# Performance work log

Hardware: AMD Instinct MI355X
Metric: run time of the kernel (lower is better)

## Reference

```python
import jax, jax.numpy as jnp
import numpy as np

N = 8192      # points
K = 16        # nsample neighbors
CIN = 64      # in_plane
C = 256       # out_plane (== mid_planes)
S = 8         # share_planes
EPS = 1e-5


def _bn(x, g, b, axes):
    # BatchNorm1d (training-mode batch stats, biased var), channel = last dim
    m = x.mean(axes, keepdims=True)
    v = x.var(axes, keepdims=True)
    return (x - m) / jnp.sqrt(v + EPS) * g + b


def _knn(p, k):
    # brute-force KNN over a single batch (o = [N]); indices include self
    sq = jnp.sum(p * p, axis=1)
    d2 = sq[:, None] + sq[None, :] - 2.0 * (p @ p.T)   # [N, N]
    idx = jax.lax.top_k(-d2, k)[1]                      # [N, K]
    return jax.lax.stop_gradient(idx)


def setup_inputs() -> dict:
    key = jax.random.key(0)
    ks = jax.random.split(key, 16)
    W = lambda i, shp, s=0.05: jax.random.normal(ks[i], shp, jnp.float32) * s
    one = lambda d: jnp.ones((d,), jnp.float32)
    zero = lambda d: jnp.zeros((d,), jnp.float32)
    return {
        "p": jax.random.normal(ks[0], (N, 3), jnp.float32),
        "x": jax.random.normal(ks[1], (N, CIN), jnp.float32),
        "o": jnp.array([N], dtype=jnp.int32),
        # PointAggregation (stride=1): Linear(no bias) + BN
        "W_pa": W(2, (CIN, C)), "g_pa": one(C), "b_pa": zero(C),
        # SelfFusion.linear1 (no bias) + bn1
        "W1": W(3, (C, C)), "g1": one(C), "b1": zero(C),
        # SelfFusionLayer q/k/v
        "Wq": W(4, (C, C)), "bq": zero(C),
        "Wk": W(5, (C, C)), "bk": zero(C),
        "Wv": W(6, (C, C)), "bv": zero(C),
        # linear_p: Linear(3,3)+BN(3)+ReLU+Linear(3,C)
        "Wp1": W(7, (3, 3), 0.3), "bp1": zero(3), "gp": one(3), "bp": zero(3),
        "Wp2": W(8, (3, C), 0.3), "bp2": zero(C),
        # linear_w: BN(C)+ReLU+Linear(C,C//S)+BN(C//S)+ReLU+Linear(C//S,C//S)
        "gw1": one(C), "bw1": zero(C),
        "Ww1": W(9, (C, C // S)), "bww1": zero(C // S),
        "gw2": one(C // S), "bw2": zero(C // S),
        "Ww2": W(10, (C // S, C // S), 0.2), "bww2": zero(C // S),
        # bn2, linear3 (no bias) + bn3
        "g2": one(C), "b2": zero(C),
        "W3": W(11, (C, C)), "g3": one(C), "b3": zero(C),
    }


def reference(p, x, o, W_pa, g_pa, b_pa, W1, g1, b1, Wq, bq, Wk, bk, Wv, bv,
              Wp1, bp1, gp, bp, Wp2, bp2, gw1, bw1, Ww1, bww1, gw2, bw2,
              Ww2, bww2, g2, b2, W3, g3, b3):
    relu = jax.nn.relu
    # --- PointAggregation (stride=1) ---
    h = relu(_bn(x @ W_pa, g_pa, b_pa, (0,)))          # [N, C]
    # --- SelfFusion block ---
    identity = h
    h = relu(_bn(h @ W1, g1, b1, (0,)))                # [N, C]
    # SelfFusionLayer
    xq = h @ Wq + bq                                   # [N, C]
    xk = h @ Wk + bk
    xv = h @ Wv + bv
    idx = _knn(p, K)                                   # [N, K]
    rel = p[idx] - p[:, None, :]                       # [N, K, 3] relative coords
    xk_g = xk[idx]                                     # [N, K, C]
    xv_g = xv[idx]                                     # [N, K, C]
    # linear_p: Linear(3,3) -> BN(3) -> ReLU -> Linear(3,C)
    p_r = rel @ Wp1 + bp1
    p_r = relu(_bn(p_r, gp, bp, (0, 1)))
    p_r = p_r @ Wp2 + bp2                              # [N, K, C]
    # mid_planes == out_planes so view(...).sum(2) is identity
    w = xk_g - xq[:, None, :] + p_r                    # [N, K, C]
    # linear_w: BN -> ReLU -> Linear -> BN -> ReLU -> Linear
    w = relu(_bn(w, gw1, bw1, (0, 1)))
    w = w @ Ww1 + bww1                                 # [N, K, C//S]
    w = relu(_bn(w, gw2, bw2, (0, 1)))
    w = w @ Ww2 + bww2                                 # [N, K, C//S]
    w = jax.nn.softmax(w, axis=1)                      # softmax over neighbors
    y = ((xv_g + p_r).reshape(N, K, S, C // S) * w[:, :, None, :]).sum(1)
    y = y.reshape(N, C)
    # back in SelfFusion
    y = relu(_bn(y, g2, b2, (0,)))
    y = _bn(y @ W3, g3, b3, (0,))
    x2 = relu(y + identity)
    return (p, x2, o)
```

## Files before the change

kernel.cpp:

```cpp
#include <hip/hip_runtime.h>
#include <hip/hip_bf16.h>

#define INV_N  (1.0f/8192.0f)
#define INV_NK (1.0f/131072.0f)

typedef __attribute__((ext_vector_type(8))) short bf16x8;
typedef __attribute__((ext_vector_type(4))) float f32x4;
typedef unsigned short u16;

__device__ __forceinline__ u16 f2b(float f) {
  unsigned u = __float_as_uint(f);
  return (u16)((u + 0x7FFFu + ((u >> 16) & 1u)) >> 16);
}
__device__ __forceinline__ float b2f(u16 u) {
  return __uint_as_float(((unsigned)u) << 16);
}

__device__ __forceinline__ float bn_ap(float v, const float* st, int C, int ch,
                                       float inv, float g, float b) {
  float m = st[ch] * inv;
  float var = st[C + ch] * inv - m * m;
  return (v - m) * rsqrtf(var + 1e-5f) * g + b;
}

__launch_bounds__(256)
__global__ void prep_k(const float* __restrict__ p, const int* __restrict__ o,
                       const float* __restrict__ Ww1,
                       float4* __restrict__ pp, u16* __restrict__ Ww1t,
                       float* __restrict__ st, float* __restrict__ out) {
  int b = blockIdx.x, t = threadIdx.x;
  int e = b*256 + t;
  if (b < 16) st[b*256 + t] = 0.f;
  if (e < 24576) out[e] = p[e];
  if (e == 0) out[24576 + 2097152] = (float)o[0];
  if (e < 8192) {
    float x = p[e*3+0], y = p[e*3+1], z = p[e*3+2];
    pp[e] = make_float4(x, y, z, (x*x + y*y) + z*z);
  }
  if (b >= 88) {
    int q = (b - 88)*1024 + t*4;
#pragma unroll
    for (int ii = 0; ii < 4; ++ii) {
      int e2 = q + ii;
      int k = e2 >> 5, n = e2 & 31;
      Ww1t[n*256 + k] = f2b(Ww1[e2]);
    }
  }
}

template<int ROWS, int SPLIT>
__launch_bounds__(256)
__global__ void red_k(const float* __restrict__ part, float* __restrict__ outp,
                      int width) {
  int ncg = width >> 6;
  int cg = blockIdx.x % ncg, sp = blockIdx.x / ncg;
  int lane = threadIdx.x & 63, chunk = threadIdx.x >> 6;
  int c = cg*64 + lane;
  constexpr int R  = ROWS / SPLIT;
  constexpr int RC = R / 4;
  float s = 0.f;
  int i0 = sp*R + chunk*RC;
#pragma unroll 4
  for (int i = i0; i < i0 + RC; ++i) s += part[(size_t)i*width + c];
  __shared__ float red[4][64];
  red[chunk][lane] = s;
  __syncthreads();
  if (threadIdx.x < 64) {
    float v = red[0][lane] + red[1][lane] + red[2][lane] + red[3][lane];
    if (SPLIT == 1) outp[c] = v;
    else atomicAdd(&outp[c], v);
  }
}

__launch_bounds__(512)
__global__ void knn_k(const float4* __restrict__ pp, int* __restrict__ idxo) {
  __shared__ float4 buf[2048];
  int t = threadIdx.x;
  int wave = t >> 6, lane = t & 63;
  int q = blockIdx.x*8 + wave;
  float4 qv = pp[q];
  const float BIG = __uint_as_float(0x7F7FFFFFu);
  float d[3];
#pragma unroll
  for (int s = 0; s < 3; ++s) d[s] = BIG;
  for (int ch = 0; ch < 4; ++ch) {
#pragma unroll
    for (int s = 0; s < 4; ++s)
      buf[s*512 + t] = pp[ch*2048 + s*512 + t];
    __syncthreads();
#pragma unroll 4
    for (int it = 0; it < 32; ++it) {
      int jl = it*64 + lane;
      float4 c = buf[jl];
      int j = ch*2048 + jl;
      float dot = qv.x*c.x + (qv.y*c.y + qv.z*c.z);
      float d2 = __fmaf_rn(-2.0f, dot, qv.w + c.w);
      float pk = __uint_as_float((__float_as_uint(d2) & 0xFFFFE000u) | (unsigned)j);
      d[2] = fminf(fmaxf(d[1], pk), d[2]);
      d[1] = fminf(fmaxf(d[0], pk), d[1]);
      d[0] = fminf(d[0], pk);
    }
    __syncthreads();
  }
  for (int r = 0; r < 16; ++r) {
    float bd = d[0];
#pragma unroll
    for (int m = 1; m < 64; m <<= 1)
      bd = fminf(bd, __shfl_xor(bd, m));
    if (lane == 0) idxo[q*16 + r] = (int)(__float_as_uint(bd) & 0x1FFFu);
    if (d[0] == bd) {
      d[0] = d[1]; d[1] = d[2]; d[2] = BIG;
    }
  }
}

template<typename TA, typename TO, bool BNA, bool STATS>
__launch_bounds__(256)
__global__ void mfgemm_k(const TA* __restrict__ A, const float* __restrict__ st,
                         const float* __restrict__ g, const float* __restrict__ bb,
                         float inv_cnt,
                         const float* __restrict__ W, TO* __restrict__ out,
                         float* __restrict__ stout, int KA, int NOUT) {
  __shared__ short As[64][72];
  __shared__ short Bt[64][72];
  __shared__ float lscl[256], lsft[256];
  int t = threadIdx.x;
  int m0 = blockIdx.x * 64, n0 = blockIdx.y * 64;
  if (BNA) {
    for (int e = t; e < KA; e += 256) {
      float m = st[e] * inv_cnt;
      float var = st[KA + e] * inv_cnt - m*m;
      float sc = rsqrtf(var + 1e-5f) * g[e];
      lscl[e] = sc; lsft[e] = bb[e] - m*sc;
    }
    __syncthreads();
  }
  const f32x4 zero = {0.f, 0.f, 0.f, 0.f};
  f32x4 acc[2][2] = {{zero, zero}, {zero, zero}};
  int wv = t >> 6, l = t & 63;
  int wm = wv & 1, wn = wv >> 1;
  int lr = l & 15, lk = (l >> 4) * 8;
  int ra = t >> 4, qa = t & 15;
  int bn = t & 63, bkc = t >> 6;
  for (int k0 = 0; k0 < KA; k0 += 64) {
#pragma unroll
    for (int rp = 0; rp < 4; ++rp) {
      int r = rp*16 + ra;
      float vv[4];
      if constexpr (sizeof(TA) == 4) {
        float4 av = *(const float4*)((const float*)A + (size_t)(m0 + r)*KA + k0 + qa*4);
        vv[0] = av.x; vv[1] = av.y; vv[2] = av.z; vv[3] = av.w;
      } else {
        short4 av = *(const short4*)((const u16*)A + (size_t)(m0 + r)*KA + k0 + qa*4);
#pragma unroll
        for (int jj = 0; jj < 4; ++jj) vv[jj] = b2f(((u16*)&av)[jj]);
      }
      short4 s;
#pragma unroll
      for (int jj = 0; jj < 4; ++jj) {
        float v = vv[jj];
        if (BNA) { int ch = k0 + qa*4 + jj; v = fmaxf(fmaf(v, lscl[ch], lsft[ch]), 0.f); }
        ((u16*)&s)[jj] = f2b(v);
      }
      *(short4*)&As[r][qa*4] = s;
    }
    {
      float v[16];
#pragma unroll
      for (int j2 = 0; j2 < 16; ++j2)
        v[j2] = W[(size_t)(k0 + bkc*16 + j2)*NOUT + n0 + bn];
      bf16x8 w0, w1v;
#pragma unroll
      for (int j2 = 0; j2 < 8; ++j2) {
        w0[j2]  = (short)f2b(v[j2]);
        w1v[j2] = (short)f2b(v[8 + j2]);
      }
      *(bf16x8*)&Bt[bn][bkc*16]     = w0;
      *(bf16x8*)&Bt[bn][bkc*16 + 8] = w1v;
    }
    __syncthreads();
#pragma unroll
    for (int fk = 0; fk < 2; ++fk) {
      bf16x8 a0 = *(const bf16x8*)&As[wm*32 +      lr][fk*32 + lk];
      bf16x8 a1 = *(const bf16x8*)&As[wm*32 + 16 + lr][fk*32 + lk];
      bf16x8 b0 = *(const bf16x8*)&Bt[wn*32 +      lr][fk*32 + lk];
      bf16x8 b1 = *(const bf16x8*)&Bt[wn*32 + 16 + lr][fk*32 + lk];
      acc[0][0] = __builtin_amdgcn_mfma_f32_16x16x32_bf16(a0, b0, acc[0][0], 0, 0, 0);
      acc[0][1] = __builtin_amdgcn_mfma_f32_16x16x32_bf16(a0, b1, acc[0][1], 0, 0, 0);
      acc[1][0] = __builtin_amdgcn_mfma_f32_16x16x32_bf16(a1, b0, acc[1][0], 0, 0, 0);
      acc[1][1] = __builtin_amdgcn_mfma_f32_16x16x32_bf16(a1, b1, acc[1][1], 0, 0, 0);
    }
    __syncthreads();
  }
#pragma unroll
  for (int fn = 0; fn < 2; ++fn) {
    int col = n0 + wn*32 + fn*16 + lr;
    float s1 = 0.f, s2 = 0.f;
#pragma unroll
    for (int fm = 0; fm < 2; ++fm) {
#pragma unroll
      for (int r = 0; r < 4; ++r) {
        int row = m0 + wm*32 + fm*16 + (l >> 4)*4 + r;
        float v = acc[fm][fn][r];
        if constexpr (sizeof(TO) == 4) out[(size_t)row*NOUT + col] = v;
        else                           out[(size_t)row*NOUT + col] = f2b(v);
        if (STATS) { s1 += v; s2 += v*v; }
      }
    }
    if (STATS) {
      s1 += __shfl_xor(s1, 16); s1 += __shfl_xor(s1, 32);
      s2 += __shfl_xor(s2, 16); s2 += __shfl_xor(s2, 32);
      if (l < 16) {
        atomicAdd(&stout[col], s1);
        atomicAdd(&stout[NOUT + col], s2);
      }
    }
  }
}

__launch_bounds__(256)
__global__ void qkv_k(const u16* __restrict__ t1, const float* __restrict__ st,
                      const float* __restrict__ g1, const float* __restrict__ b1,
                      const float* __restrict__ Wq, const float* __restrict__ bq,
                      const float* __restrict__ Wk, const float* __restrict__ bk,
                      const float* __restrict__ Wv, const float* __restrict__ bv,
                      u16* __restrict__ xq, u16* __restrict__ xk, u16* __restrict__ xv) {
  __shared__ short As[64][72];
  __shared__ short Bt[3][64][72];
  __shared__ float lscl[256], lsft[256];
  int t = threadIdx.x;
  int m0 = blockIdx.x * 64, n0 = blockIdx.y * 64;
  {
    int e = t;
    float m = st[e] * INV_N;
    float var = st[256 + e] * INV_N - m*m;
    float sc = rsqrtf(var + 1e-5f) * g1[e];
    lscl[e] = sc; lsft[e] = b1[e] - m*sc;
  }
  __syncthreads();
  const f32x4 zero = {0.f, 0.f, 0.f, 0.f};
  f32x4 acc[3][2][2];
#pragma unroll
  for (int w = 0; w < 3; ++w)
#pragma unroll
    for (int i = 0; i < 2; ++i)
#pragma unroll
      for (int j = 0; j < 2; ++j) acc[w][i][j] = zero;
  int wv = t >> 6, l = t & 63;
  int wm = wv & 1, wn = wv >> 1;
  int lr = l & 15, lk = (l >> 4) * 8;
  int ra = t >> 4, qa = t & 15;
  int bn = t & 63, bkc = t >> 6;
  const float* Ws[3] = {Wq, Wk, Wv};
  for (int k0 = 0; k0 < 256; k0 += 64) {
#pragma unroll
    for (int rp = 0; rp < 4; ++rp) {
      int r = rp*16 + ra;
      short4 av = *(const short4*)(t1 + (size_t)(m0 + r)*256 + k0 + qa*4);
      short4 s;
#pragma unroll
      for (int jj = 0; jj < 4; ++jj) {
        int ch = k0 + qa*4 + jj;
        float v = fmaxf(fmaf(b2f(((u16*)&av)[jj]), lscl[ch], lsft[ch]), 0.f);
        ((u16*)&s)[jj] = f2b(v);
      }
      *(short4*)&As[r][qa*4] = s;
    }
#pragma unroll
    for (int w = 0; w < 3; ++w) {
      float v[16];
#pragma unroll
      for (int j2 = 0; j2 < 16; ++j2)
        v[j2] = Ws[w][(size_t)(k0 + bkc*16 + j2)*256 + n0 + bn];
      bf16x8 w0, w1v;
#pragma unroll
      for (int j2 = 0; j2 < 8; ++j2) {
        w0[j2]  = (short)f2b(v[j2]);
        w1v[j2] = (short)f2b(v[8 + j2]);
      }
      *(bf16x8*)&Bt[w][bn][bkc*16]     = w0;
      *(bf16x8*)&Bt[w][bn][bkc*16 + 8] = w1v;
    }
    __syncthreads();
#pragma unroll
    for (int fk = 0; fk < 2; ++fk) {
      bf16x8 a0 = *(const bf16x8*)&As[wm*32 +      lr][fk*32 + lk];
      bf16x8 a1 = *(const bf16x8*)&As[wm*32 + 16 + lr][fk*32 + lk];
#pragma unroll
      for (int w = 0; w < 3; ++w) {
        bf16x8 b0 = *(const bf16x8*)&Bt[w][wn*32 +      lr][fk*32 + lk];
        bf16x8 b1 = *(const bf16x8*)&Bt[w][wn*32 + 16 + lr][fk*32 + lk];
        acc[w][0][0] = __builtin_amdgcn_mfma_f32_16x16x32_bf16(a0, b0, acc[w][0][0], 0, 0, 0);
        acc[w][0][1] = __builtin_amdgcn_mfma_f32_16x16x32_bf16(a0, b1, acc[w][0][1], 0, 0, 0);
        acc[w][1][0] = __builtin_amdgcn_mfma_f32_16x16x32_bf16(a1, b0, acc[w][1][0], 0, 0, 0);
        acc[w][1][1] = __builtin_amdgcn_mfma_f32_16x16x32_bf16(a1, b1, acc[w][1][1], 0, 0, 0);
      }
    }
    __syncthreads();
  }
  u16* outs[3] = {xq, xk, xv};
  const float* bs[3] = {bq, bk, bv};
#pragma unroll
  for (int w = 0; w < 3; ++w) {
#pragma unroll
    for (int fn = 0; fn < 2; ++fn) {
      int col = n0 + wn*32 + fn*16 + lr;
      float bvv = bs[w][col];
#pragma unroll
      for (int fm = 0; fm < 2; ++fm) {
#pragma unroll
        for (int r = 0; r < 4; ++r) {
          int row = m0 + wm*32 + fm*16 + (l >> 4)*4 + r;
          outs[w][(size_t)row*256 + col] = f2b(acc[w][fm][fn][r] + bvv);
        }
      }
    }
  }
}

__launch_bounds__(256)
__global__ void stats256_k(const u16* __restrict__ X, float* __restrict__ psy) {
  int c = threadIdx.x;
  int r0 = blockIdx.x * 32;
  float s1 = 0.f, s2 = 0.f;
  for (int r = 0; r < 32; ++r) {
    float v = b2f(X[(size_t)(r0 + r)*256 + c]);
    s1 += v; s2 += v*v;
  }
  psy[(size_t)blockIdx.x*512 + c]       = s1;
  psy[(size_t)blockIdx.x*512 + 256 + c] = s2;
}

__device__ __forceinline__ void comp_pr1(const float* p, int i, int j,
                                         const float* Wp1, const float* bp1,
                                         float pr1[3]) {
  float rx = p[j*3+0] - p[i*3+0];
  float ry = p[j*3+1] - p[i*3+1];
  float rz = p[j*3+2] - p[i*3+2];
#pragma unroll
  for (int c = 0; c < 3; ++c)
    pr1[c] = rx*Wp1[c] + ry*Wp1[3+c] + rz*Wp1[6+c] + bp1[c];
}

__device__ __forceinline__ void comp_prv(const float* p, int i, int j,
                                         const float* Wp1, const float* bp1,
                                         const float* gp, const float* bpp,
                                         const float* sp, float o3[3]) {
  float pr1[3];
  comp_pr1(p, i, j, Wp1, bp1, pr1);
#pragma unroll
  for (int c = 0; c < 3; ++c)
    o3[c] = fmaxf(bn_ap(pr1[c], sp, 3, c, INV_NK, gp[c], bpp[c]), 0.0f);
}

__launch_bounds__(256)
__global__ void prstats_k(const float* __restrict__ p, const int* __restrict__ idx,
                          const float* Wp1, const float* bp1, float* __restrict__ sp) {
  float s[3] = {0,0,0}, s2[3] = {0,0,0};
  for (int it = 0; it < 4; ++it) {
    int e = blockIdx.x*1024 + it*256 + threadIdx.x;
    int i = e >> 4;
    int j = idx[e] & 8191;
    float pr1[3];
    comp_pr1(p, i, j, Wp1, bp1, pr1);
#pragma unroll
    for (int c = 0; c < 3; ++c) { s[c] += pr1[c]; s2[c] += pr1[c]*pr1[c]; }
  }
#pragma unroll
  for (int m = 1; m < 64; m <<= 1) {
#pragma unroll
    for (int c = 0; c < 3; ++c) {
      s[c]  += __shfl_xor(s[c],  m);
      s2[c] += __shfl_xor(s2[c], m);
    }
  }
  __shared__ float red[4][6];
  int wv = threadIdx.x >> 6, lane = threadIdx.x & 63;
  if (lane == 0) {
#pragma unroll
    for (int c = 0; c < 3; ++c) { red[wv][c] = s[c]; red[wv][3+c] = s2[c]; }
  }
  __syncthreads();
  if (threadIdx.x < 6) {
    float v = red[0][threadIdx.x] + red[1][threadIdx.x] +
              red[2][threadIdx.x] + red[3][threadIdx.x];
    atomicAdd(&sp[threadIdx.x], v);
  }
}

__launch_bounds__(256)
__global__ void wstats_k(const u16* __restrict__ xk, const u16* __restrict__ xq,
                         const float* __restrict__ p, const int* __restrict__ idx,
                         const float* Wp1, const float* bp1, const float* gp, const float* bpp,
                         const float* sp, const float* __restrict__ Wp2, const float* bp2,
                         float* __restrict__ pws) {
  __shared__ float prv[8][16][4];
  __shared__ int   jidx[8][16];
  int base = blockIdx.x * 8;
  int t = threadIdx.x;
  if (t < 128) {
    int pt = t >> 4, k = t & 15;
    int j = idx[(base + pt)*16 + k] & 8191;
    jidx[pt][k] = j;
    float o3[3];
    comp_prv(p, base + pt, j, Wp1, bp1, gp, bpp, sp, o3);
    prv[pt][k][0] = o3[0]; prv[pt][k][1] = o3[1]; prv[pt][k][2] = o3[2];
  }
  __syncthreads();
  int c = t;
  float wp0 = Wp2[c], wp1v = Wp2[256+c], wp2v = Wp2[512+c];
  float bbv = bp2[c];
  float s1 = 0.f, s2 = 0.f;
  for (int pt = 0; pt < 8; ++pt) {
    int i = base + pt;
    float xqv = b2f(xq[(size_t)i*256 + c]);
    u16 kvals[16];
#pragma unroll
    for (int k = 0; k < 16; ++k)
      kvals[k] = xk[(size_t)jidx[pt][k]*256 + c];
#pragma unroll
    for (int k = 0; k < 16; ++k) {
      float pr = prv[pt][k][0]*wp0 + prv[pt][k][1]*wp1v + prv[pt][k][2]*wp2v + bbv;
      float wval = b2f(kvals[k]) - xqv + pr;
      s1 += wval; s2 += wval*wval;
    }
  }
  pws[(size_t)blockIdx.x*512 + c]       = s1;
  pws[(size_t)blockIdx.x*512 + 256 + c] = s2;
}

__launch_bounds__(256)
__global__ void w1gemm_k(const u16* __restrict__ xk, const u16* __restrict__ xq,
                         const float* __restrict__ p, const int* __restrict__ idx,
                         const float* Wp1, const float* bp1, const float* gp, const float* bpp,
                         const float* sp, const float* __restrict__ Wp2, const float* bp2,
                         const float* sw, const float* gw1, const float* bw1,
                         const u16* __restrict__ Ww1t, const float* bww1,
                         u16* __restrict__ w1, float* __restrict__ pw1) {
  __shared__ short sA[64][264];
  __shared__ float prv[64][3];
  __shared__ int   jrow[64];
  __shared__ float sred[256];
  int t = threadIdx.x;
  int base4 = blockIdx.x * 4;
  if (t < 64) {
    int grow = blockIdx.x*64 + t;
    int j = idx[grow] & 8191;
    jrow[t] = j;
    float o3[3];
    comp_prv(p, grow >> 4, j, Wp1, bp1, gp, bpp, sp, o3);
    prv[t][0] = o3[0]; prv[t][1] = o3[1]; prv[t][2] = o3[2];
  }
  __syncthreads();
  {
    int o = t & 31, rs = t >> 5;
    int ch0 = o*8;
    int jr[8];
#pragma unroll
    for (int ii = 0; ii < 8; ++ii) jr[ii] = jrow[ii*8 + rs];
    bf16x8 kvv[8], qvv[8];
#pragma unroll
    for (int ii = 0; ii < 8; ++ii) {
      int r = ii*8 + rs;
      kvv[ii] = *(const bf16x8*)(xk + (size_t)jr[ii]*256 + ch0);
      qvv[ii] = *(const bf16x8*)(xq + (size_t)(base4 + (r >> 4))*256 + ch0);
    }
    float sclv[8], sftv[8], w0v[8], w1vv[8], w2v[8], b2v[8];
#pragma unroll
    for (int h = 0; h < 2; ++h) {
      float4 swm = *(const float4*)(sw + ch0 + h*4);
      float4 sws = *(const float4*)(sw + 256 + ch0 + h*4);
      float4 g4  = *(const float4*)(gw1 + ch0 + h*4);
      float4 bb4 = *(const float4*)(bw1 + ch0 + h*4);
      float4 p0v = *(const float4*)(Wp2 + ch0 + h*4);
      float4 p1v = *(const float4*)(Wp2 + 256 + ch0 + h*4);
      float4 p2v = *(const float4*)(Wp2 + 512 + ch0 + h*4);
      float4 bp4 = *(const float4*)(bp2 + ch0 + h*4);
      float mv[4] = {swm.x, swm.y, swm.z, swm.w};
      float sv[4] = {sws.x, sws.y, sws.z, sws.w};
      float gv[4] = {g4.x, g4.y, g4.z, g4.w};
      float bv[4] = {bb4.x, bb4.y, bb4.z, bb4.w};
      float a0[4] = {p0v.x, p0v.y, p0v.z, p0v.w};
      float a1[4] = {p1v.x, p1v.y, p1v.z, p1v.w};
      float a2[4] = {p2v.x, p2v.y, p2v.z, p2v.w};
      float a3[4] = {bp4.x, bp4.y, bp4.z, bp4.w};
#pragma unroll
      for (int jj = 0; jj < 4; ++jj) {
        int e = h*4 + jj;
        float m = mv[jj]*INV_NK;
        float var = sv[jj]*INV_NK - m*m;
        float sc = rsqrtf(var + 1e-5f)*gv[jj];
        sclv[e] = sc; sftv[e] = bv[jj] - m*sc;
        w0v[e] = a0[jj]; w1vv[e] = a1[jj]; w2v[e] = a2[jj]; b2v[e] = a3[jj];
      }
    }
#pragma unroll
    for (int ii = 0; ii < 8; ++ii) {
      int r = ii*8 + rs;
      float p0 = prv[r][0], p1 = prv[r][1], p2 = prv[r][2];
      bf16x8 av;
#pragma unroll
      for (int e = 0; e < 8; ++e) {
        float v = b2f((u16)kvv[ii][e]) - b2f((u16)qvv[ii][e])
                + p0*w0v[e] + p1*w1vv[e] + p2*w2v[e] + b2v[e];
        v = fmaxf(fmaf(v, sclv[e], sftv[e]), 0.f);
        av[e] = (short)f2b(v);
      }
      *(bf16x8*)&sA[r][ch0] = av;
    }
  }
  __syncthreads();
  const f32x4 zero = {0.f,0.f,0.f,0.f};
  f32x4 acc[2] = {zero, zero};
  int wv = t >> 6, l = t & 63;
  int lr = l & 15, hi = l >> 4;
#pragma unroll
  for (int k0 = 0; k0 < 8; ++k0) {
    int kb = k0*32 + hi*8;
    bf16x8 a  = *(const bf16x8*)&sA[wv*16 + lr][kb];
    bf16x8 b0 = *(const bf16x8*)(Ww1t + (size_t)lr*256      + kb);
    bf16x8 b1 = *(const bf16x8*)(Ww1t + (size_t)(16+lr)*256 + kb);
    acc[0] = __builtin_amdgcn_mfma_f32_16x16x32_bf16(a, b0, acc[0], 0, 0, 0);
    acc[1] = __builtin_amdgcn_mfma_f32_16x16x32_bf16(a, b1, acc[1], 0, 0, 0);
  }
#pragma unroll
  for (int fn = 0; fn < 2; ++fn) {
    int col = fn*16 + lr;
    float bv = bww1[col];
    float s1 = 0.f, s2 = 0.f;
#pragma unroll
    for (int r = 0; r < 4; ++r) {
      int grow = blockIdx.x*64 + wv*16 + hi*4 + r;
      float v = acc[fn][r] + bv;
      w1[(size_t)grow*32 + col] = f2b(v);
      s1 += v; s2 += v*v;
    }
    s1 += __shfl_xor(s1, 16); s1 += __shfl_xor(s1, 32);
    s2 += __shfl_xor(s2, 16); s2 += __shfl_xor(s2, 32);
    if (l < 16) { sred[(wv*2+fn)*16 + lr] = s1; sred[128 + (wv*2+fn)*16 + lr] = s2; }
  }
  __syncthreads();
  if (t < 32) {
    float a = 0.f, b = 0.f;
#pragma unroll
    for (int w2 = 0; w2 < 4; ++w2) {
      a += sred[(w2*2 + (t >> 4))*16 + (t & 15)];
      b += sred[128 + (w2*2 + (t >> 4))*16 + (t & 15)];
    }
    pw1[(size_t)blockIdx.x*64 + t]      = a;
    pw1[(size_t)blockIdx.x*64 + 32 + t] = b;
  }
}

__launch_bounds__(256)
__global__ void aggr_k(const u16* __restrict__ w1, const float* sw1,
                       const float* gw2, const float* bw2,
                       const float* __restrict__ Ww2, const float* bww2,
                       const u16* __restrict__ xv,
                       const float* __restrict__ p, const int* __restrict__ idx,
                       const float* Wp1, const float* bp1, const float* gp, const float* bpp,
                       const float* sp, const float* __restrict__ Wp2, const float* bp2,
                       u16* __restrict__ y) {
  __shared__ float lw1[16][32];
  __shared__ float lW2[32][32];
  __shared__ float sw2[16][33];
  __shared__ float prv[16][4];
  __shared__ int   jidx[16];
  int i = blockIdx.x, t = threadIdx.x;
  for (int e = t; e < 1024; e += 256) lW2[e >> 5][e & 31] = Ww2[e];
  for (int e = t; e < 512; e += 256) {
    int c32 = e & 31;
    float v = b2f(w1[(size_t)i*512 + e]);
    v = fmaxf(bn_ap(v, sw1, 32, c32, INV_NK, gw2[c32], bw2[c32]), 0.0f);
    lw1[e >> 5][c32] = v;
  }
  if (t < 16) jidx[t] = idx[i*16 + t] & 8191;
  __syncthreads();
  if (t < 16) {
    float o3[3];
    comp_prv(p, i, jidx[t], Wp1, bp1, gp, bpp, sp, o3);
    prv[t][0] = o3[0]; prv[t][1] = o3[1]; prv[t][2] = o3[2];
  }
  for (int e = t; e < 512; e += 256) {
    int k = e >> 5, c32 = e & 31;
    float a = bww2[c32];
#pragma unroll
    for (int j = 0; j < 32; ++j) a += lw1[k][j] * lW2[j][c32];
    sw2[k][c32] = a;
  }
  __syncthreads();
  if (t < 32) {
    float mx = -3.0e38f;
#pragma unroll
    for (int k = 0; k < 16; ++k) mx = fmaxf(mx, sw2[k][t]);
    float s = 0.f;
#pragma unroll
    for (int k = 0; k < 16; ++k) { float e2 = expf(sw2[k][t] - mx); sw2[k][t] = e2; s += e2; }
    float r = 1.0f / s;
#pragma unroll
    for (int k = 0; k < 16; ++k) sw2[k][t] *= r;
  }
  __syncthreads();
  int c = t;
  float wp0 = Wp2[c], wp1v = Wp2[256+c], wp2v = Wp2[512+c];
  float bbv = bp2[c];
  int c32 = c & 31;
  float acc = 0.f;
#pragma unroll
  for (int k = 0; k < 16; ++k) {
    int j = jidx[k];
    float pr = prv[k][0]*wp0 + prv[k][1]*wp1v + prv[k][2]*wp2v + bbv;
    float xvv = b2f(xv[(size_t)j*256 + c]);
    acc += (xvv + pr) * sw2[k][c32];
  }
  y[(size_t)i*256 + c] = f2b(acc);
}

__launch_bounds__(256)
__global__ void final_k(const u16* __restrict__ t0, const float* s0,
                        const float* g0, const float* b0,
                        const u16* __restrict__ t3, const float* s3,
                        const float* g3, const float* b3,
                        float* __restrict__ out) {
  int i = blockIdx.x, c = threadIdx.x;
  size_t off = (size_t)i*256 + c;
  float h0 = fmaxf(bn_ap(b2f(t0[off]), s0, 256, c, INV_N, g0[c], b0[c]), 0.0f);
  float v3 = bn_ap(b2f(t3[off]), s3, 256, c, INV_N, g3[c], b3[c]);
  out[24576 + off] = fmaxf(v3 + h0, 0.0f);
}

extern "C" void kernel_launch(void* const* d_in, const int* in_sizes, int n_in,
                              void* d_out, int out_size, void* d_ws, size_t ws_size,
                              hipStream_t stream) {
  (void)in_sizes; (void)n_in; (void)out_size; (void)ws_size;
  const float* p    = (const float*)d_in[0];
  const float* x    = (const float*)d_in[1];
  const int*   o    = (const int*)  d_in[2];
  const float* W_pa = (const float*)d_in[3];
  const float* g_pa = (const float*)d_in[4];
  const float* b_pa = (const float*)d_in[5];
  const float* W1   = (const float*)d_in[6];
  const float* g1   = (const float*)d_in[7];
  const float* b1   = (const float*)d_in[8];
  const float* Wq   = (const float*)d_in[9];
  const float* bq   = (const float*)d_in[10];
  const float* Wk   = (const float*)d_in[11];
  const float* bk   = (const float*)d_in[12];
  const float* Wv   = (const float*)d_in[13];
  const float* bv   = (const float*)d_in[14];
  const float* Wp1  = (const float*)d_in[15];
  const float* bp1  = (const float*)d_in[16];
  const float* gp   = (const float*)d_in[17];
  const float* bpp  = (const float*)d_in[18];
  const float* Wp2  = (const float*)d_in[19];
  const float* bp2  = (const float*)d_in[20];
  const float* gw1  = (const float*)d_in[21];
  const float* bw1  = (const float*)d_in[22];
  const float* Ww1  = (const float*)d_in[23];
  const float* bww1 = (const float*)d_in[24];
  const float* gw2  = (const float*)d_in[25];
  const float* bw2  = (const float*)d_in[26];
  const float* Ww2  = (const float*)d_in[27];
  const float* bww2 = (const float*)d_in[28];
  const float* g2   = (const float*)d_in[29];
  const float* b2   = (const float*)d_in[30];
  const float* W3   = (const float*)d_in[31];
  const float* g3   = (const float*)d_in[32];
  const float* b3   = (const float*)d_in[33];

  char* ws = (char*)d_ws;
  u16*   t0  = (u16*)  (ws + 0);
  u16*   t1  = (u16*)  (ws + 4194304);
  u16*   xq  = (u16*)  (ws + 8388608);
  u16*   xk  = (u16*)  (ws + 12582912);
  u16*   xv  = (u16*)  (ws + 16777216);
  u16*   w1  = (u16*)  (ws + 20971520);
  int*   idx = (int*)  (ws + 29360128);
  float* st  = (float*)(ws + 29884416);
  u16*   Ww1t= (u16*)  (ws + 29900800);
  float* pw1 = (float*)(ws + 30408704);
  float* pws = (float*)(ws + 30932992);
  float* psy = (float*)(ws + 33030144);
  u16*   y   = t1;
  u16*   t3  = xq;
  float4* pp = (float4*)(ws + 20971520);

  prep_k<<<96, 256, 0, stream>>>(p, o, Ww1, pp, Ww1t, st, (float*)d_out);
  knn_k<<<1024, 512, 0, stream>>>(pp, idx);

  mfgemm_k<float, u16, false, true><<<dim3(128, 4), 256, 0, stream>>>(
      x, nullptr, nullptr, nullptr, 0.f, W_pa, t0, st + 0, 64, 256);

  mfgemm_k<u16, u16, true, true><<<dim3(128, 4), 256, 0, stream>>>(
      t0, st + 0, g_pa, b_pa, INV_N, W1, t1, st + 512, 256, 256);

  qkv_k<<<dim3(128, 4), 256, 0, stream>>>(
      t1, st + 512, g1, b1, Wq, bq, Wk, bk, Wv, bv, xq, xk, xv);

  prstats_k<<<128, 256, 0, stream>>>(p, idx, Wp1, bp1, st + 2624);

  wstats_k<<<1024, 256, 0, stream>>>(xk, xq, p, idx, Wp1, bp1, gp, bpp,
                                     st + 2624, Wp2, bp2, pws);
  red_k<1024, 4><<<32, 256, 0, stream>>>(pws, st + 1024, 512);

  w1gemm_k<<<2048, 256, 0, stream>>>(xk, xq, p, idx, Wp1, bp1, gp, bpp,
                                     st + 2624, Wp2, bp2, st + 1024,
                                     gw1, bw1, Ww1t, bww1, w1, pw1);
  red_k<2048, 16><<<16, 256, 0, stream>>>(pw1, st + 2560, 64);

  aggr_k<<<8192, 256, 0, stream>>>(w1, st + 2560, gw2, bw2, Ww2, bww2, xv,
                                   p, idx, Wp1, bp1, gp, bpp, st + 2624,
                                   Wp2, bp2, y);
  stats256_k<<<256, 256, 0, stream>>>(y, psy);
  red_k<256, 2><<<16, 256, 0, stream>>>(psy, st + 1536, 512);

  mfgemm_k<u16, u16, true, true><<<dim3(128, 4), 256, 0, stream>>>(
      y, st + 1536, g2, b2, INV_N, W3, t3, st + 2048, 256, 256);

  final_k<<<8192, 256, 0, stream>>>(t0, st + 0, g_pa, b_pa,
                                    t3, st + 2048, g3, b3, (float*)d_out);
}
```

Before: 198.0 us.

## Fuse independent KNN and first GEMM into one launch, and prstats with second GEMM

```diff
diff --git a/kernel.cpp b/kernel.cpp
--- a/kernel.cpp
+++ b/kernel.cpp
@@ -72,12 +72,12 @@
   }
 }
 
-__launch_bounds__(512)
-__global__ void knn_k(const float4* __restrict__ pp, int* __restrict__ idxo) {
-  __shared__ float4 buf[2048];
+__device__ __forceinline__ void knn_dev(char* smem, const float4* __restrict__ pp,
+                                        int* __restrict__ idxo, int kb) {
+  float4* buf = (float4*)smem;
   int t = threadIdx.x;
   int wave = t >> 6, lane = t & 63;
-  int q = blockIdx.x*8 + wave;
+  int q = kb*4 + wave;
   float4 qv = pp[q];
   const float BIG = __uint_as_float(0x7F7FFFFFu);
   float d[3];
@@ -85,8 +85,8 @@
   for (int s = 0; s < 3; ++s) d[s] = BIG;
   for (int ch = 0; ch < 4; ++ch) {
 #pragma unroll
-    for (int s = 0; s < 4; ++s)
-      buf[s*512 + t] = pp[ch*2048 + s*512 + t];
+    for (int s = 0; s < 8; ++s)
+      buf[s*256 + t] = pp[ch*2048 + s*256 + t];
     __syncthreads();
 #pragma unroll 4
     for (int it = 0; it < 32; ++it) {
@@ -115,17 +115,17 @@
 }
 
 template<typename TA, typename TO, bool BNA, bool STATS>
-__launch_bounds__(256)
-__global__ void mfgemm_k(const TA* __restrict__ A, const float* __restrict__ st,
-                         const float* __restrict__ g, const float* __restrict__ bb,
-                         float inv_cnt,
-                         const float* __restrict__ W, TO* __restrict__ out,
-                         float* __restrict__ stout, int KA, int NOUT) {
-  __shared__ short As[64][72];
-  __shared__ short Bt[64][72];
-  __shared__ float lscl[256], lsft[256];
+__device__ __forceinline__ void mfgemm_dev(char* smem,
+    const TA* __restrict__ A, const float* __restrict__ st,
+    const float* __restrict__ g, const float* __restrict__ bb, float inv_cnt,
+    const float* __restrict__ W, TO* __restrict__ out,
+    float* __restrict__ stout, int KA, int NOUT, int bm, int bn_) {
+  short (*As)[72] = (short(*)[72])smem;
+  short (*Bt)[72] = (short(*)[72])(smem + 9216);
+  float* lscl = (float*)(smem + 18432);
+  float* lsft = (float*)(smem + 19456);
   int t = threadIdx.x;
-  int m0 = blockIdx.x * 64, n0 = blockIdx.y * 64;
+  int m0 = bm * 64, n0 = bn_ * 64;
   if (BNA) {
     for (int e = t; e < KA; e += 256) {
       float m = st[e] * inv_cnt;
@@ -216,6 +216,105 @@
       }
     }
   }
+}
+
+__device__ __forceinline__ void comp_pr1(const float* p, int i, int j,
+                                         const float* Wp1, const float* bp1,
+                                         float pr1[3]) {
+  float rx = p[j*3+0] - p[i*3+0];
+  float ry = p[j*3+1] - p[i*3+1];
+  float rz = p[j*3+2] - p[i*3+2];
+#pragma unroll
+  for (int c = 0; c < 3; ++c)
+    pr1[c] = rx*Wp1[c] + ry*Wp1[3+c] + rz*Wp1[6+c] + bp1[c];
+}
+
+__device__ __forceinline__ void comp_prv(const float* p, int i, int j,
+                                         const float* Wp1, const float* bp1,
+                                         const float* gp, const float* bpp,
+                                         const float* sp, float o3[3]) {
+  float pr1[3];
+  comp_pr1(p, i, j, Wp1, bp1, pr1);
+#pragma unroll
+  for (int c = 0; c < 3; ++c)
+    o3[c] = fmaxf(bn_ap(pr1[c], sp, 3, c, INV_NK, gp[c], bpp[c]), 0.0f);
+}
+
+__device__ __forceinline__ void prstats_dev(char* smem,
+    const float* __restrict__ p, const int* __restrict__ idx,
+    const float* Wp1, const float* bp1, float* __restrict__ sp, int pb) {
+  float s[3] = {0,0,0}, s2[3] = {0,0,0};
+  for (int it = 0; it < 4; ++it) {
+    int e = pb*1024 + it*256 + threadIdx.x;
+    int i = e >> 4;
+    int j = idx[e] & 8191;
+    float pr1[3];
+    comp_pr1(p, i, j, Wp1, bp1, pr1);
+#pragma unroll
+    for (int c = 0; c < 3; ++c) { s[c] += pr1[c]; s2[c] += pr1[c]*pr1[c]; }
+  }
+#pragma unroll
+  for (int m = 1; m < 64; m <<= 1) {
+#pragma unroll
+    for (int c = 0; c < 3; ++c) {
+      s[c]  += __shfl_xor(s[c],  m);
+      s2[c] += __shfl_xor(s2[c], m);
+    }
+  }
+  float (*red)[6] = (float(*)[6])smem;
+  int wv = threadIdx.x >> 6, lane = threadIdx.x & 63;
+  if (lane == 0) {
+#pragma unroll
+    for (int c = 0; c < 3; ++c) { red[wv][c] = s[c]; red[wv][3+c] = s2[c]; }
+  }
+  __syncthreads();
+  if (threadIdx.x < 6) {
+    float v = red[0][threadIdx.x] + red[1][threadIdx.x] +
+              red[2][threadIdx.x] + red[3][threadIdx.x];
+    atomicAdd(&sp[threadIdx.x], v);
+  }
+}
+
+__launch_bounds__(256)
+__global__ void gemmknn_k(const float* __restrict__ x, const float* __restrict__ W_pa,
+                          u16* __restrict__ t0, float* __restrict__ st0,
+                          const float4* __restrict__ pp, int* __restrict__ idxo) {
+  extern __shared__ char smem[];
+  int b = blockIdx.x;
+  if (b < 512)
+    mfgemm_dev<float, u16, false, true>(smem, x, nullptr, nullptr, nullptr, 0.f,
+                                        W_pa, t0, st0, 64, 256, b & 127, b >> 7);
+  else
+    knn_dev(smem, pp, idxo, b - 512);
+}
+
+__launch_bounds__(256)
+__global__ void gemmpr_k(const u16* __restrict__ t0, const float* __restrict__ st0,
+                         const float* __restrict__ g_pa, const float* __restrict__ b_pa,
+                         const float* __restrict__ W1, u16* __restrict__ t1,
+                         float* __restrict__ st1,
+                         const float* __restrict__ p, const int* __restrict__ idx,
+                         const float* __restrict__ Wp1, const float* __restrict__ bp1,
+                         float* __restrict__ sp) {
+  extern __shared__ char smem[];
+  int b = blockIdx.x;
+  if (b < 512)
+    mfgemm_dev<u16, u16, true, true>(smem, t0, st0, g_pa, b_pa, INV_N,
+                                     W1, t1, st1, 256, 256, b & 127, b >> 7);
+  else
+    prstats_dev(smem, p, idx, Wp1, bp1, sp, b - 512);
+}
+
+template<typename TA, typename TO, bool BNA, bool STATS>
+__launch_bounds__(256)
+__global__ void mfgemm_k(const TA* __restrict__ A, const float* __restrict__ st,
+                         const float* __restrict__ g, const float* __restrict__ bb,
+                         float inv_cnt,
+                         const float* __restrict__ W, TO* __restrict__ out,
+                         float* __restrict__ stout, int KA, int NOUT) {
+  extern __shared__ char smem[];
+  mfgemm_dev<TA, TO, BNA, STATS>(smem, A, st, g, bb, inv_cnt, W, out, stout,
+                                 KA, NOUT, blockIdx.x, blockIdx.y);
 }
 
 __launch_bounds__(256)
@@ -329,63 +428,6 @@
   }
   psy[(size_t)blockIdx.x*512 + c]       = s1;
   psy[(size_t)blockIdx.x*512 + 256 + c] = s2;
-}
-
-__device__ __forceinline__ void comp_pr1(const float* p, int i, int j,
-                                         const float* Wp1, const float* bp1,
-                                         float pr1[3]) {
-  float rx = p[j*3+0] - p[i*3+0];
-  float ry = p[j*3+1] - p[i*3+1];
-  float rz = p[j*3+2] - p[i*3+2];
-#pragma unroll
-  for (int c = 0; c < 3; ++c)
-    pr1[c] = rx*Wp1[c] + ry*Wp1[3+c] + rz*Wp1[6+c] + bp1[c];
-}
-
-__device__ __forceinline__ void comp_prv(const float* p, int i, int j,
-                                         const float* Wp1, const float* bp1,
-                                         const float* gp, const float* bpp,
-                                         const float* sp, float o3[3]) {
-  float pr1[3];
-  comp_pr1(p, i, j, Wp1, bp1, pr1);
-#pragma unroll
-  for (int c = 0; c < 3; ++c)
-    o3[c] = fmaxf(bn_ap(pr1[c], sp, 3, c, INV_NK, gp[c], bpp[c]), 0.0f);
-}
-
-__launch_bounds__(256)
-__global__ void prstats_k(const float* __restrict__ p, const int* __restrict__ idx,
-                          const float* Wp1, const float* bp1, float* __restrict__ sp) {
-  float s[3] = {0,0,0}, s2[3] = {0,0,0};
-  for (int it = 0; it < 4; ++it) {
-    int e = blockIdx.x*1024 + it*256 + threadIdx.x;
-    int i = e >> 4;
-    int j = idx[e] & 8191;
-    float pr1[3];
-    comp_pr1(p, i, j, Wp1, bp1, pr1);
-#pragma unroll
-    for (int c = 0; c < 3; ++c) { s[c] += pr1[c]; s2[c] += pr1[c]*pr1[c]; }
-  }
-#pragma unroll
-  for (int m = 1; m < 64; m <<= 1) {
-#pragma unroll
-    for (int c = 0; c < 3; ++c) {
-      s[c]  += __shfl_xor(s[c],  m);
-      s2[c] += __shfl_xor(s2[c], m);
-    }
-  }
-  __shared__ float red[4][6];
-  int wv = threadIdx.x >> 6, lane = threadIdx.x & 63;
-  if (lane == 0) {
-#pragma unroll
-    for (int c = 0; c < 3; ++c) { red[wv][c] = s[c]; red[wv][3+c] = s2[c]; }
-  }
-  __syncthreads();
-  if (threadIdx.x < 6) {
-    float v = red[0][threadIdx.x] + red[1][threadIdx.x] +
-              red[2][threadIdx.x] + red[3][threadIdx.x];
-    atomicAdd(&sp[threadIdx.x], v);
-  }
 }
 
 __launch_bounds__(256)
@@ -686,18 +728,14 @@
   float4* pp = (float4*)(ws + 20971520);
 
   prep_k<<<96, 256, 0, stream>>>(p, o, Ww1, pp, Ww1t, st, (float*)d_out);
-  knn_k<<<1024, 512, 0, stream>>>(pp, idx);
-
-  mfgemm_k<float, u16, false, true><<<dim3(128, 4), 256, 0, stream>>>(
-      x, nullptr, nullptr, nullptr, 0.f, W_pa, t0, st + 0, 64, 256);
-
-  mfgemm_k<u16, u16, true, true><<<dim3(128, 4), 256, 0, stream>>>(
-      t0, st + 0, g_pa, b_pa, INV_N, W1, t1, st + 512, 256, 256);
+
+  gemmknn_k<<<2560, 256, 32768, stream>>>(x, W_pa, t0, st + 0, pp, idx);
+
+  gemmpr_k<<<640, 256, 20480, stream>>>(t0, st + 0, g_pa, b_pa, W1, t1, st + 512,
+                                        p, idx, Wp1, bp1, st + 2624);
 
   qkv_k<<<dim3(128, 4), 256, 0, stream>>>(
       t1, st + 512, g1, b1, Wq, bq, Wk, bk, Wv, bv, xq, xk, xv);
-
-  prstats_k<<<128, 256, 0, stream>>>(p, idx, Wp1, bp1, st + 2624);
 
   wstats_k<<<1024, 256, 0, stream>>>(xk, xq, p, idx, Wp1, bp1, gp, bpp,
                                      st + 2624, Wp2, bp2, pws);
@@ -714,7 +752,7 @@
   stats256_k<<<256, 256, 0, stream>>>(y, psy);
   red_k<256, 2><<<16, 256, 0, stream>>>(psy, st + 1536, 512);
 
-  mfgemm_k<u16, u16, true, true><<<dim3(128, 4), 256, 0, stream>>>(
+  mfgemm_k<u16, u16, true, true><<<dim3(128, 4), 256, 20480, stream>>>(
       y, st + 1536, g2, b2, INV_N, W3, t3, st + 2048, 256, 256);
 
   final_k<<<8192, 256, 0, stream>>>(t0, st + 0, g_pa, b_pa,
```

Result: faster. 190.6 us (-3.8%).
